# Performance work log

Hardware: AMD Instinct MI355X
Metric: run time of the kernel (lower is better)

The kernel has to match this reference:

```python
import jax, jax.numpy as jnp
import numpy as np


def _gcn_conv(x, edge_index, W, b):
    """Faithful PyG GCNConv: add self-loops, symmetric norm, scatter-sum, bias."""
    n = x.shape[0]
    loop = jnp.arange(n, dtype=edge_index.dtype)
    src = jnp.concatenate([edge_index[0], loop])  # [E+n]
    dst = jnp.concatenate([edge_index[1], loop])
    # in-degree at dst (edge_weight = 1), as in gcn_norm
    deg = jax.ops.segment_sum(jnp.ones(src.shape[0], x.dtype), dst, num_segments=n)
    dinv = jnp.where(deg > 0, jax.lax.rsqrt(deg), 0.0)
    norm = dinv[src] * dinv[dst]                  # [E+n]
    h = x @ W                                     # [n, C] small GEMM
    msg = h[src] * norm[:, None]                  # gather + scale (dominant traffic)
    out = jax.ops.segment_sum(msg, dst, num_segments=n)  # scatter-sum
    return out + b


def setup_inputs() -> dict:
    key = jax.random.key(0)
    ks = jax.random.split(key, 8)
    N, E, C = 50000, 1000000, 64
    scale = 1.0 / np.sqrt(C)
    return {
        "x_star": jax.random.normal(ks[0], (N, C), jnp.float32),
        "x_gal": jax.random.normal(ks[1], (N, C), jnp.float32),
        "edge_ss_near": jax.random.randint(ks[2], (2, E), 0, N, jnp.int64),
        "edge_ss_far": jax.random.randint(ks[3], (2, E), 0, N, jnp.int64),
        "edge_gg_near": jax.random.randint(ks[4], (2, E), 0, N, jnp.int64),
        "W_ss_near": jax.random.normal(ks[5], (C, C), jnp.float32) * scale,
        "W_ss_far": jax.random.normal(ks[6], (C, C), jnp.float32) * scale,
        "W_gg_near": jax.random.normal(ks[7], (C, C), jnp.float32) * scale,
        "b_ss_near": jnp.zeros((C,), jnp.float32),
        "b_ss_far": jnp.zeros((C,), jnp.float32),
        "b_gg_near": jnp.zeros((C,), jnp.float32),
    }


def reference(x_star, x_gal, edge_ss_near, edge_ss_far, edge_gg_near,
              W_ss_near, W_ss_far, W_gg_near,
              b_ss_near, b_ss_far, b_gg_near):
    # HeteroConv with aggr='sum': per-edge-type GCNConv, summed per dst node type.
    out_star = (_gcn_conv(x_star, edge_ss_near, W_ss_near, b_ss_near)
                + _gcn_conv(x_star, edge_ss_far, W_ss_far, b_ss_far))
    out_gal = _gcn_conv(x_gal, edge_gg_near, W_gg_near, b_gg_near)
    return out_star, out_gal
```

## Files before the change

kernel.cpp:

```cpp
#include <hip/hip_runtime.h>
#include <hip/hip_fp16.h>

#define CCH 64
#define RPB 32
#define PCH 4096
#define NBMAX 1568
#define GR 64
#define SG 4
#define STCAP 4096

typedef int int4a __attribute__((ext_vector_type(4), aligned(4)));

__global__ void __launch_bounds__(256) k_hist(const int* __restrict__ e0,
        const int* __restrict__ e1, const int* __restrict__ e2,
        int* __restrict__ H, int E, int NB, int NBLK) {
    int c = blockIdx.y;
    const int* dd = ((c == 0) ? e0 : (c == 1) ? e1 : e2) + E;
    int base = blockIdx.x * PCH;
    int nE = E - base; if (nE > PCH) nE = PCH;
    __shared__ int hist[NBMAX];
    int t = threadIdx.x;
    for (int i = t; i < NB; i += 256) hist[i] = 0;
    __syncthreads();
    for (int k = t * 4; k < nE; k += 1024) {
        if (k + 3 < nE) {
            int4a d = *(const int4a*)(dd + base + k);
            atomicAdd(&hist[d.x >> 5], 1); atomicAdd(&hist[d.y >> 5], 1);
            atomicAdd(&hist[d.z >> 5], 1); atomicAdd(&hist[d.w >> 5], 1);
        } else {
            for (int j = k; j < nE; ++j) atomicAdd(&hist[dd[base + j] >> 5], 1);
        }
    }
    __syncthreads();
    int* Hrow = H + ((size_t)c * NBLK + blockIdx.x) * NB;
    for (int i = t; i < NB; i += 256) Hrow[i] = hist[i];
}

__global__ void __launch_bounds__(256) k_colscan(int* __restrict__ H,
        int* __restrict__ colsum, int NB, int NBLK) {
    int c = blockIdx.y;
    int b = blockIdx.x * 4 + (threadIdx.x >> 6);
    if (b >= NB) return;
    int l = threadIdx.x & 63;
    int* Hc = H + (size_t)c * NBLK * NB;
    int run = 0;
    for (int c0 = 0; c0 < NBLK; c0 += 64) {
        int blk = c0 + l;
        int v = (blk < NBLK) ? Hc[(size_t)blk * NB + b] : 0;
        int s = v;
        #pragma unroll
        for (int off = 1; off < 64; off <<= 1) {
            int u = __shfl_up(s, off, 64);
            if (l >= off) s += u;
        }
        if (blk < NBLK) Hc[(size_t)blk * NB + b] = run + s - v;
        run += __shfl(s, 63, 64);
    }
    if (l == 0) colsum[c * NB + b] = run;
}

__global__ void __launch_bounds__(1024) k_bscan(const int* __restrict__ colsum,
        int* __restrict__ bstart, __half* __restrict__ zrow, int NB, int E) {
    int c = blockIdx.x, t = threadIdx.x;
    if (c == 0 && t < 32) ((float*)zrow)[t] = 0.f;
    __shared__ int sm[1024];
    int i0 = 2 * t, i1 = 2 * t + 1;
    int v0 = (i0 < NB) ? colsum[c * NB + i0] : 0;
    int v1 = (i1 < NB) ? colsum[c * NB + i1] : 0;
    sm[t] = v0 + v1;
    __syncthreads();
    #pragma unroll
    for (int off = 1; off < 1024; off <<= 1) {
        int u = (t >= off) ? sm[t - off] : 0;
        __syncthreads();
        sm[t] += u;
        __syncthreads();
    }
    int ex = sm[t] - (v0 + v1);
    if (i0 < NB) bstart[c * (NB + 1) + i0] = ex;
    if (i1 < NB) bstart[c * (NB + 1) + i1] = ex + v0;
    if (t == 0) bstart[c * (NB + 1) + NB] = E;
}

__global__ void __launch_bounds__(256) k_part2(const int* __restrict__ e0,
        const int* __restrict__ e1, const int* __restrict__ e2,
        const int* __restrict__ H, const int* __restrict__ colsum,
        const int* __restrict__ bstart,
        unsigned* __restrict__ bdata, int E, int NB, int NBLK) {
    int c = blockIdx.y;
    const int* ed = (c == 0) ? e0 : (c == 1) ? e1 : e2;
    int base = blockIdx.x * PCH;
    int nE = E - base; if (nE > PCH) nE = PCH;
    __shared__ unsigned staged[PCH];
    __shared__ int hist[NBMAX];
    __shared__ int off[NBMAX];
    __shared__ int sm[256];
    int t = threadIdx.x;
    const int* Hcur = H + ((size_t)c * NBLK + blockIdx.x) * NB;
    const int* Hnxt = (blockIdx.x == NBLK - 1) ? (colsum + c * NB)
                                               : (Hcur + NB);
    const int* bs = bstart + c * (NB + 1);
    for (int i = t; i < NB; i += 256) {
        int cu = Hcur[i];
        off[i] = bs[i] + cu;
        hist[i] = Hnxt[i] - cu;
    }
    __syncthreads();
    int C = (NB + 255) >> 8;
    int lo = t * C, hi = lo + C; if (hi > NB) hi = NB; if (lo > NB) lo = NB;
    int s = 0;
    for (int i = lo; i < hi; ++i) s += hist[i];
    sm[t] = s;
    __syncthreads();
    #pragma unroll
    for (int o = 1; o < 256; o <<= 1) {
        int u = (t >= o) ? sm[t - o] : 0;
        __syncthreads();
        sm[t] += u;
        __syncthreads();
    }
    int run = (t == 0) ? 0 : sm[t - 1];
    for (int i = lo; i < hi; ++i) {
        int h = hist[i];
        off[i] -= run;
        hist[i] = run;
        run += h;
    }
    __syncthreads();
    for (int k = t * 4; k < nE; k += 1024) {
        if (k + 3 < nE) {
            int4a s4 = *(const int4a*)(ed + base + k);
            int4a d4 = *(const int4a*)(ed + E + base + k);
            int sl;
            sl = atomicAdd(&hist[d4.x >> 5], 1); staged[sl] = (unsigned)s4.x | ((unsigned)d4.x << 16);
            sl = atomicAdd(&hist[d4.y >> 5], 1); staged[sl] = (unsigned)s4.y | ((unsigned)d4.y << 16);
            sl = atomicAdd(&hist[d4.z >> 5], 1); staged[sl] = (unsigned)s4.z | ((unsigned)d4.z << 16);
            sl = atomicAdd(&hist[d4.w >> 5], 1); staged[sl] = (unsigned)s4.w | ((unsigned)d4.w << 16);
        } else {
            for (int j = k; j < nE; ++j) {
                int s0 = ed[base + j];
                int d0 = ed[E + base + j];
                int sl = atomicAdd(&hist[d0 >> 5], 1);
                staged[sl] = (unsigned)s0 | ((unsigned)d0 << 16);
            }
        }
    }
    __syncthreads();
    unsigned* bo = bdata + (size_t)c * E;
    for (int sI = t; sI < nE; sI += 256) {
        unsigned rec = staged[sI];
        int b = (int)(rec >> 16) >> 5;
        bo[off[b] + sI] = rec;
    }
}

__global__ void __launch_bounds__(256) k_sort32(const unsigned* __restrict__ bdata,
        const int* __restrict__ bstart, int* __restrict__ sdat,
        int* __restrict__ rs, float* __restrict__ dinv, int E, int N, int NB) {
    int c = blockIdx.y;
    int b0 = blockIdx.x * SG;
    __shared__ unsigned staged[STCAP];
    __shared__ int cnt[SG * RPB];
    __shared__ int cur[SG * RPB];
    __shared__ int sb[SG + 1];
    int t = threadIdx.x;
    if (t < SG * RPB) cnt[t] = 0;
    if (t <= SG) {
        int b = b0 + t; if (b > NB) b = NB;
        sb[t] = bstart[c * (NB + 1) + b];
    }
    __syncthreads();
    int s0 = sb[0], sE = sb[SG];
    int n = sE - s0;
    const unsigned* bd = bdata + (size_t)c * E;
    bool fits = (n <= STCAP);
    if (fits) {
        for (int i = t; i < n; i += 256) staged[i] = bd[s0 + i];
        __syncthreads();
        for (int i = t; i < n; i += 256) {
            int dst = (int)(staged[i] >> 16);
            atomicAdd(&cnt[((dst >> 5) - b0) * RPB + (dst & 31)], 1);
        }
    } else {
        for (int i = s0 + t; i < sE; i += 256) {
            int dst = (int)(bd[i] >> 16);
            atomicAdd(&cnt[((dst >> 5) - b0) * RPB + (dst & 31)], 1);
        }
    }
    __syncthreads();
    if (t < SG * RPB) {
        int v = cnt[t];
        int s = v;
        #pragma unroll
        for (int off = 1; off < RPB; off <<= 1) {
            int u = __shfl_up(s, off, RPB);
            if ((t & (RPB - 1)) >= off) s += u;
        }
        int g = t >> 5, r = t & 31;
        int ex = sb[g] + s - v;
        cur[t] = ex;
        int row = (b0 + g) * RPB + r;
        if (b0 + g < NB && row < N) {
            rs[c * (N + 1) + row] = ex;
            dinv[c * N + row] = rsqrtf((float)(v + 1));
        }
    }
    if (blockIdx.x == 0 && t == 0) rs[c * (N + 1) + N] = E;
    __syncthreads();
    int* so = sdat + (size_t)c * E;
    if (fits) {
        for (int i = t; i < n; i += 256) {
            unsigned r = staged[i];
            int dst = (int)(r >> 16);
            int slot = atomicAdd(&cur[((dst >> 5) - b0) * RPB + (dst & 31)], 1);
            so[slot] = (int)(r & 0xFFFFu);
        }
    } else {
        for (int i = s0 + t; i < sE; i += 256) {
            unsigned r = bd[i];
            int dst = (int)(r >> 16);
            int slot = atomicAdd(&cur[((dst >> 5) - b0) * RPB + (dst & 31)], 1);
            so[slot] = (int)(r & 0xFFFFu);
        }
    }
}

__global__ void __launch_bounds__(256) k_gemm_all(const float* __restrict__ xs_,
        const float* __restrict__ xg_, const float* __restrict__ W0,
        const float* __restrict__ W1, const float* __restrict__ W2,
        const float* __restrict__ dinv, __half* __restrict__ h16, int N) {
    int star = (blockIdx.y == 0);
    const float* x = star ? xs_ : xg_;
    __shared__ float Ws[2][CCH * CCH];
    __shared__ float xT[CCH * (GR + 1)];
    int t = threadIdx.x;
    int row0 = blockIdx.x * GR;
    size_t NC = (size_t)N * CCH;
    if (star) {
        #pragma unroll
        for (int j = 0; j < 4; ++j) {
            int idx = j * 1024 + t * 4;
            *(float4*)(&Ws[0][idx]) = *(const float4*)(W0 + idx);
            *(float4*)(&Ws[1][idx]) = *(const float4*)(W1 + idx);
        }
    } else {
        #pragma unroll
        for (int j = 0; j < 4; ++j) {
            int idx = j * 1024 + t * 4;
            *(float4*)(&Ws[0][idx]) = *(const float4*)(W2 + idx);
        }
    }
    #pragma unroll
    for (int j = 0; j < 4; ++j) {
        int idx = t + j * 256;
        int r = idx >> 4;
        int c0 = (idx & 15) * 4;
        int row = row0 + r;
        float4 v = make_float4(0.f, 0.f, 0.f, 0.f);
        if (row < N) v = *(const float4*)(x + (size_t)row * CCH + c0);
        xT[(c0 + 0) * (GR + 1) + r] = v.x;
        xT[(c0 + 1) * (GR + 1) + r] = v.y;
        xT[(c0 + 2) * (GR + 1) + r] = v.z;
        xT[(c0 + 3) * (GR + 1) + r] = v.w;
    }
    __syncthreads();
    int c4 = (t & 15) * 4;
    int r0 = (t >> 4) * 4;
    if (star) {
        float4 a0 = make_float4(0.f, 0.f, 0.f, 0.f), a1 = a0, a2 = a0, a3 = a0;
        float4 d0 = a0, d1 = a0, d2 = a0, d3 = a0;
        #pragma unroll 4
        for (int k = 0; k < CCH; ++k) {
            float4 wv = *(float4*)(&Ws[0][k * CCH + c4]);
            float4 uv = *(float4*)(&Ws[1][k * CCH + c4]);
            float x0 = xT[k * (GR + 1) + r0 + 0];
            float x1 = xT[k * (GR + 1) + r0 + 1];
            float x2 = xT[k * (GR + 1) + r0 + 2];
            float x3 = xT[k * (GR + 1) + r0 + 3];
            a0.x += x0 * wv.x; a0.y += x0 * wv.y; a0.z += x0 * wv.z; a0.w += x0 * wv.w;
            a1.x += x1 * wv.x; a1.y += x1 * wv.y; a1.z += x1 * wv.z; a1.w += x1 * wv.w;
            a2.x += x2 * wv.x; a2.y += x2 * wv.y; a2.z += x2 * wv.z; a2.w += x2 * wv.w;
            a3.x += x3 * wv.x; a3.y += x3 * wv.y; a3.z += x3 * wv.z; a3.w += x3 * wv.w;
            d0.x += x0 * uv.x; d0.y += x0 * uv.y; d0.z += x0 * uv.z; d0.w += x0 * uv.w;
            d1.x += x1 * uv.x; d1.y += x1 * uv.y; d1.z += x1 * uv.z; d1.w += x1 * uv.w;
            d2.x += x2 * uv.x; d2.y += x2 * uv.y; d2.z += x2 * uv.z; d2.w += x2 * uv.w;
            d3.x += x3 * uv.x; d3.y += x3 * uv.y; d3.z += x3 * uv.z; d3.w += x3 * uv.w;
        }
        float4 av[4] = {a0, a1, a2, a3};
        float4 dv4[4] = {d0, d1, d2, d3};
        #pragma unroll
        for (int i = 0; i < 4; ++i) {
            int row = row0 + r0 + i;
            if (row < N) {
                float dd0 = dinv[row];
                float dd1 = dinv[N + row];
                union { __half2 h2[2]; float2 f2; } u;
                u.h2[0] = __floats2half2_rn(av[i].x * dd0, av[i].y * dd0);
                u.h2[1] = __floats2half2_rn(av[i].z * dd0, av[i].w * dd0);
                *(float2*)(h16 + (size_t)row * CCH + c4) = u.f2;
                u.h2[0] = __floats2half2_rn(dv4[i].x * dd1, dv4[i].y * dd1);
                u.h2[1] = __floats2half2_rn(dv4[i].z * dd1, dv4[i].w * dd1);
                *(float2*)(h16 + NC + (size_t)row * CCH + c4) = u.f2;
            }
        }
    } else {
        float4 a0 = make_float4(0.f, 0.f, 0.f, 0.f), a1 = a0, a2 = a0, a3 = a0;
        #pragma unroll 8
        for (int k = 0; k < CCH; ++k) {
            float4 wv = *(float4*)(&Ws[0][k * CCH + c4]);
            float x0 = xT[k * (GR + 1) + r0 + 0];
            float x1 = xT[k * (GR + 1) + r0 + 1];
            float x2 = xT[k * (GR + 1) + r0 + 2];
            float x3 = xT[k * (GR + 1) + r0 + 3];
            a0.x += x0 * wv.x; a0.y += x0 * wv.y; a0.z += x0 * wv.z; a0.w += x0 * wv.w;
            a1.x += x1 * wv.x; a1.y += x1 * wv.y; a1.z += x1 * wv.z; a1.w += x1 * wv.w;
            a2.x += x2 * wv.x; a2.y += x2 * wv.y; a2.z += x2 * wv.z; a2.w += x2 * wv.w;
            a3.x += x3 * wv.x; a3.y += x3 * wv.y; a3.z += x3 * wv.z; a3.w += x3 * wv.w;
        }
        float4 av[4] = {a0, a1, a2, a3};
        #pragma unroll
        for (int i = 0; i < 4; ++i) {
            int row = row0 + r0 + i;
            if (row < N) {
                float dd = dinv[2 * N + row];
                union { __half2 h2[2]; float2 f2; } u;
                u.h2[0] = __floats2half2_rn(av[i].x * dd, av[i].y * dd);
                u.h2[1] = __floats2half2_rn(av[i].z * dd, av[i].w * dd);
                *(float2*)(h16 + 2 * NC + (size_t)row * CCH + c4) = u.f2;
            }
        }
    }
}

__device__ __forceinline__ float4 gat4p(const __half* __restrict__ p, int l16) {
    union { float2 f2; __half2 h2[2]; } u;
    u.f2 = ((const float2*)p)[l16];
    float2 a = __half22float2(u.h2[0]);
    float2 b = __half22float2(u.h2[1]);
    return make_float4(a.x, a.y, b.x, b.y);
}

__device__ __forceinline__ void acc4(float4& a, float4 v) {
    a.x += v.x; a.y += v.y; a.z += v.z; a.w += v.w;
}

__global__ void __launch_bounds__(256) k_pull(const int* __restrict__ rs,
        const int* __restrict__ sdat, const __half* __restrict__ h16,
        const float* __restrict__ dinv, const __half* __restrict__ zrow,
        const float* __restrict__ b0, const float* __restrict__ b1,
        const float* __restrict__ b2,
        float* __restrict__ out, int N, int E) {
    int row = blockIdx.x * 4 + (threadIdx.x >> 6);
    if (row >= 2 * N) return;
    int lane = threadIdx.x & 63;
    int q = lane >> 4;
    int l16 = lane & 15;
    size_t NC = (size_t)N * CCH;

    const __half* hcL;
    const int* sdL;
    int beg, end;
    float ddL;
    float4 bias;
    float* op;
    float4 acc = make_float4(0.f, 0.f, 0.f, 0.f);
    if (row < N) {
        int cv = q >> 1;
        const int* rsA = rs + cv * (N + 1);
        int bg = rsA[row], eg = rsA[row + 1];
        int mid = (bg + eg) >> 1;
        beg = (q & 1) ? mid : bg;
        end = (q & 1) ? eg : mid;
        hcL = h16 + (size_t)cv * NC;
        sdL = sdat + (size_t)cv * E;
        ddL = dinv[cv * N + row];
        if (!(q & 1)) acc = gat4p(hcL + (size_t)row * CCH, l16);
        float4 bv0 = ((const float4*)b0)[l16];
        float4 bv1 = ((const float4*)b1)[l16];
        bias = make_float4(bv0.x + bv1.x, bv0.y + bv1.y,
                           bv0.z + bv1.z, bv0.w + bv1.w);
        op = out + (size_t)row * CCH;
    } else {
        int r = row - N;
        const int* rs2 = rs + 2 * (N + 1);
        int bg = rs2[r], eg = rs2[r + 1];
        int len = eg - bg;
        beg = bg + ((len * q) >> 2);
        end = bg + ((len * (q + 1)) >> 2);
        hcL = h16 + 2 * NC;
        sdL = sdat + 2 * (size_t)E;
        ddL = dinv[2 * N + r];
        if (q == 0) acc = gat4p(hcL + (size_t)r * CCH, l16);
        bias = ((const float4*)b2)[l16];
        op = out + NC + (size_t)r * CCH;
    }

    int i = beg;
    for (; i + 7 < end; i += 8) {
        int4a q0 = *(const int4a*)(sdL + i);
        int4a q1 = *(const int4a*)(sdL + i + 4);
        float4 v0 = gat4p(hcL + (size_t)q0.x * CCH, l16);
        float4 v1 = gat4p(hcL + (size_t)q0.y * CCH, l16);
        float4 v2 = gat4p(hcL + (size_t)q0.z * CCH, l16);
        float4 v3 = gat4p(hcL + (size_t)q0.w * CCH, l16);
        float4 v4 = gat4p(hcL + (size_t)q1.x * CCH, l16);
        float4 v5 = gat4p(hcL + (size_t)q1.y * CCH, l16);
        float4 v6 = gat4p(hcL + (size_t)q1.z * CCH, l16);
        float4 v7 = gat4p(hcL + (size_t)q1.w * CCH, l16);
        acc4(acc, v0); acc4(acc, v1); acc4(acc, v2); acc4(acc, v3);
        acc4(acc, v4); acc4(acc, v5); acc4(acc, v6); acc4(acc, v7);
    }
    if (i < end) {
        int4a q0 = *(const int4a*)(sdL + i);
        int4a q1 = *(const int4a*)(sdL + i + 4);
        const __half* p0 = hcL + (size_t)q0.x * CCH;
        const __half* p1 = (i + 1 < end) ? hcL + (size_t)q0.y * CCH : zrow;
        const __half* p2 = (i + 2 < end) ? hcL + (size_t)q0.z * CCH : zrow;
        const __half* p3 = (i + 3 < end) ? hcL + (size_t)q0.w * CCH : zrow;
        const __half* p4 = (i + 4 < end) ? hcL + (size_t)q1.x * CCH : zrow;
        const __half* p5 = (i + 5 < end) ? hcL + (size_t)q1.y * CCH : zrow;
        const __half* p6 = (i + 6 < end) ? hcL + (size_t)q1.z * CCH : zrow;
        const __half* p7 = (i + 7 < end) ? hcL + (size_t)q1.w * CCH : zrow;
        float4 v0 = gat4p(p0, l16);
        float4 v1 = gat4p(p1, l16);
        float4 v2 = gat4p(p2, l16);
        float4 v3 = gat4p(p3, l16);
        float4 v4 = gat4p(p4, l16);
        float4 v5 = gat4p(p5, l16);
        float4 v6 = gat4p(p6, l16);
        float4 v7 = gat4p(p7, l16);
        acc4(acc, v0); acc4(acc, v1); acc4(acc, v2); acc4(acc, v3);
        acc4(acc, v4); acc4(acc, v5); acc4(acc, v6); acc4(acc, v7);
    }

    float4 t;
    t.x = acc.x * ddL; t.y = acc.y * ddL; t.z = acc.z * ddL; t.w = acc.w * ddL;
    t.x += __shfl_xor(t.x, 16, 64); t.y += __shfl_xor(t.y, 16, 64);
    t.z += __shfl_xor(t.z, 16, 64); t.w += __shfl_xor(t.w, 16, 64);
    t.x += __shfl_xor(t.x, 32, 64); t.y += __shfl_xor(t.y, 32, 64);
    t.z += __shfl_xor(t.z, 32, 64); t.w += __shfl_xor(t.w, 32, 64);
    if (lane < 16) {
        t.x += bias.x; t.y += bias.y; t.z += bias.z; t.w += bias.w;
        ((float4*)op)[l16] = t;
    }
}

static inline size_t align256(size_t x) { return (x + 255) & ~(size_t)255; }

extern "C" void kernel_launch(void* const* d_in, const int* in_sizes, int n_in,
                              void* d_out, int out_size, void* d_ws, size_t ws_size,
                              hipStream_t stream) {
    const float* x_star = (const float*)d_in[0];
    const float* x_gal  = (const float*)d_in[1];
    const int*   e_ssn  = (const int*)d_in[2];
    const int*   e_ssf  = (const int*)d_in[3];
    const int*   e_ggn  = (const int*)d_in[4];
    const float* W_ssn  = (const float*)d_in[5];
    const float* W_ssf  = (const float*)d_in[6];
    const float* W_ggn  = (const float*)d_in[7];
    const float* b_ssn  = (const float*)d_in[8];
    const float* b_ssf  = (const float*)d_in[9];
    const float* b_ggn  = (const float*)d_in[10];

    const int N  = in_sizes[0] / CCH;
    const int E  = in_sizes[2] / 2;
    const size_t NC = (size_t)N * CCH;
    const int NB   = (N + RPB - 1) / RPB;
    const int NBLK = (E + PCH - 1) / PCH;

    char* w = (char*)d_ws;
    __half*   h16    = (__half*)w;   w += align256((size_t)3 * NC * 2);
    float*    dinv   = (float*)w;    w += align256((size_t)3 * N * 4);
    unsigned* bdata  = (unsigned*)w; w += align256((size_t)3 * E * 4);
    int*      sdat   = (int*)w;      w += align256((size_t)3 * E * 4);
    int*      H      = (int*)w;      w += align256((size_t)3 * NBLK * NB * 4);
    int*      colsum = (int*)w;      w += align256((size_t)3 * NB * 4);
    int*      bstart = (int*)w;      w += align256((size_t)3 * (NB + 1) * 4);
    int*      rs     = (int*)w;      w += align256((size_t)3 * (N + 1) * 4);
    __half*   zrow   = (__half*)w;   w += align256((size_t)CCH * 2);

    const int B = 256;

    k_hist<<<dim3(NBLK, 3), B, 0, stream>>>(e_ssn, e_ssf, e_ggn, H, E, NB, NBLK);
    k_colscan<<<dim3((NB + 3) / 4, 3), B, 0, stream>>>(H, colsum, NB, NBLK);
    k_bscan<<<3, 1024, 0, stream>>>(colsum, bstart, zrow, NB, E);
    k_part2<<<dim3(NBLK, 3), B, 0, stream>>>(e_ssn, e_ssf, e_ggn, H, colsum,
                                             bstart, bdata, E, NB, NBLK);
    k_sort32<<<dim3((NB + SG - 1) / SG, 3), B, 0, stream>>>(bdata, bstart, sdat,
                                                            rs, dinv, E, N, NB);
    k_gemm_all<<<dim3((N + GR - 1) / GR, 2), B, 0, stream>>>(x_star, x_gal,
                                                             W_ssn, W_ssf, W_ggn,
                                                             dinv, h16, N);
    k_pull<<<(2 * N + 3) / 4, B, 0, stream>>>(rs, sdat, h16, dinv, zrow,
                                              b_ssn, b_ssf, b_ggn,
                                              (float*)d_out, N, E);
}
```

Baseline: 237.7 us.

## Replace two-level bucket sort CSR build with global-atomic counting sort

The multi-kernel CSR construction (per-chunk bucket histograms, column scans, a partition pass and a per-bucket local sort) is replaced by a direct counting sort. Per-row in-degrees are counted with global atomics, scanned into row starts, and each edge's source is then scattered into its slot through global atomic cursors. This drops the intermediate bdata buffer, the large H histogram matrix and two kernel launches. In exchange it relies on heavily contended global atomics and scattered global writes, and the order of edges within a row becomes nondeterministic.

```diff
diff --git a/kernel.cpp b/kernel.cpp
--- a/kernel.cpp
+++ b/kernel.cpp
@@ -3,70 +3,48 @@
 
 #define CCH 64
 #define RPB 32
-#define PCH 4096
-#define NBMAX 1568
+#define PCH 8192
 #define GR 64
-#define SG 4
-#define STCAP 4096
 
 typedef int int4a __attribute__((ext_vector_type(4), aligned(4)));
 
-__global__ void __launch_bounds__(256) k_hist(const int* __restrict__ e0,
+__global__ void __launch_bounds__(256) k_cnt(const int* __restrict__ e0,
         const int* __restrict__ e1, const int* __restrict__ e2,
-        int* __restrict__ H, int E, int NB, int NBLK) {
+        int* __restrict__ rcnt, int E, int N) {
     int c = blockIdx.y;
     const int* dd = ((c == 0) ? e0 : (c == 1) ? e1 : e2) + E;
+    int* rc = rcnt + (size_t)c * N;
     int base = blockIdx.x * PCH;
     int nE = E - base; if (nE > PCH) nE = PCH;
-    __shared__ int hist[NBMAX];
     int t = threadIdx.x;
-    for (int i = t; i < NB; i += 256) hist[i] = 0;
-    __syncthreads();
     for (int k = t * 4; k < nE; k += 1024) {
         if (k + 3 < nE) {
             int4a d = *(const int4a*)(dd + base + k);
-            atomicAdd(&hist[d.x >> 5], 1); atomicAdd(&hist[d.y >> 5], 1);
-            atomicAdd(&hist[d.z >> 5], 1); atomicAdd(&hist[d.w >> 5], 1);
+            atomicAdd(&rc[d.x], 1); atomicAdd(&rc[d.y], 1);
+            atomicAdd(&rc[d.z], 1); atomicAdd(&rc[d.w], 1);
         } else {
-            for (int j = k; j < nE; ++j) atomicAdd(&hist[dd[base + j] >> 5], 1);
-        }
-    }
-    __syncthreads();
-    int* Hrow = H + ((size_t)c * NBLK + blockIdx.x) * NB;
-    for (int i = t; i < NB; i += 256) Hrow[i] = hist[i];
-}
-
-__global__ void __launch_bounds__(256) k_colscan(int* __restrict__ H,
-        int* __restrict__ colsum, int NB, int NBLK) {
-    int c = blockIdx.y;
-    int b = blockIdx.x * 4 + (threadIdx.x >> 6);
-    if (b >= NB) return;
-    int l = threadIdx.x & 63;
-    int* Hc = H + (size_t)c * NBLK * NB;
-    int run = 0;
-    for (int c0 = 0; c0 < NBLK; c0 += 64) {
-        int blk = c0 + l;
-        int v = (blk < NBLK) ? Hc[(size_t)blk * NB + b] : 0;
-        int s = v;
-        #pragma unroll
-        for (int off = 1; off < 64; off <<= 1) {
-            int u = __shfl_up(s, off, 64);
-            if (l >= off) s += u;
-        }
-        if (blk < NBLK) Hc[(size_t)blk * NB + b] = run + s - v;
-        run += __shfl(s, 63, 64);
-    }
-    if (l == 0) colsum[c * NB + b] = run;
-}
-
-__global__ void __launch_bounds__(1024) k_bscan(const int* __restrict__ colsum,
-        int* __restrict__ bstart, __half* __restrict__ zrow, int NB, int E) {
+            for (int j = k; j < nE; ++j) atomicAdd(&rc[dd[base + j]], 1);
+        }
+    }
+}
+
+__global__ void __launch_bounds__(1024) k_bscan(const int* __restrict__ rcnt,
+        int* __restrict__ bstart, __half* __restrict__ zrow,
+        int NB, int N, int E) {
     int c = blockIdx.x, t = threadIdx.x;
     if (c == 0 && t < 32) ((float*)zrow)[t] = 0.f;
     __shared__ int sm[1024];
+    const int* rc = rcnt + (size_t)c * N;
     int i0 = 2 * t, i1 = 2 * t + 1;
-    int v0 = (i0 < NB) ? colsum[c * NB + i0] : 0;
-    int v1 = (i1 < NB) ? colsum[c * NB + i1] : 0;
+    int v0 = 0, v1 = 0;
+    if (i0 < NB) {
+        int r0 = i0 * RPB, hi = r0 + RPB; if (hi > N) hi = N;
+        for (int r = r0; r < hi; ++r) v0 += rc[r];
+    }
+    if (i1 < NB) {
+        int r0 = i1 * RPB, hi = r0 + RPB; if (hi > N) hi = N;
+        for (int r = r0; r < hi; ++r) v1 += rc[r];
+    }
     sm[t] = v0 + v1;
     __syncthreads();
     #pragma unroll
@@ -82,145 +60,53 @@
     if (t == 0) bstart[c * (NB + 1) + NB] = E;
 }
 
-__global__ void __launch_bounds__(256) k_part2(const int* __restrict__ e0,
+__global__ void __launch_bounds__(256) k_rs(const int* __restrict__ rcnt,
+        const int* __restrict__ bstart, int* __restrict__ rs,
+        int* __restrict__ cursor, float* __restrict__ dinv,
+        int N, int NB, int E) {
+    int c = blockIdx.y;
+    int row = blockIdx.x * 256 + threadIdx.x;
+    int l = threadIdx.x & 31;
+    int v = (row < N) ? rcnt[(size_t)c * N + row] : 0;
+    int s = v;
+    #pragma unroll
+    for (int off = 1; off < RPB; off <<= 1) {
+        int u = __shfl_up(s, off, RPB);
+        if (l >= off) s += u;
+    }
+    if (row < N) {
+        int ex = bstart[c * (NB + 1) + (row >> 5)] + s - v;
+        rs[c * (N + 1) + row] = ex;
+        cursor[(size_t)c * N + row] = ex;
+        dinv[(size_t)c * N + row] = rsqrtf((float)(v + 1));
+    }
+    if (blockIdx.x == 0 && threadIdx.x == 0) rs[c * (N + 1) + N] = E;
+}
+
+__global__ void __launch_bounds__(256) k_scat(const int* __restrict__ e0,
         const int* __restrict__ e1, const int* __restrict__ e2,
-        const int* __restrict__ H, const int* __restrict__ colsum,
-        const int* __restrict__ bstart,
-        unsigned* __restrict__ bdata, int E, int NB, int NBLK) {
+        int* __restrict__ cursor, int* __restrict__ sdat, int E, int N) {
     int c = blockIdx.y;
     const int* ed = (c == 0) ? e0 : (c == 1) ? e1 : e2;
+    int* cur = cursor + (size_t)c * N;
+    int* so = sdat + (size_t)c * E;
     int base = blockIdx.x * PCH;
     int nE = E - base; if (nE > PCH) nE = PCH;
-    __shared__ unsigned staged[PCH];
-    __shared__ int hist[NBMAX];
-    __shared__ int off[NBMAX];
-    __shared__ int sm[256];
     int t = threadIdx.x;
-    const int* Hcur = H + ((size_t)c * NBLK + blockIdx.x) * NB;
-    const int* Hnxt = (blockIdx.x == NBLK - 1) ? (colsum + c * NB)
-                                               : (Hcur + NB);
-    const int* bs = bstart + c * (NB + 1);
-    for (int i = t; i < NB; i += 256) {
-        int cu = Hcur[i];
-        off[i] = bs[i] + cu;
-        hist[i] = Hnxt[i] - cu;
-    }
-    __syncthreads();
-    int C = (NB + 255) >> 8;
-    int lo = t * C, hi = lo + C; if (hi > NB) hi = NB; if (lo > NB) lo = NB;
-    int s = 0;
-    for (int i = lo; i < hi; ++i) s += hist[i];
-    sm[t] = s;
-    __syncthreads();
-    #pragma unroll
-    for (int o = 1; o < 256; o <<= 1) {
-        int u = (t >= o) ? sm[t - o] : 0;
-        __syncthreads();
-        sm[t] += u;
-        __syncthreads();
-    }
-    int run = (t == 0) ? 0 : sm[t - 1];
-    for (int i = lo; i < hi; ++i) {
-        int h = hist[i];
-        off[i] -= run;
-        hist[i] = run;
-        run += h;
-    }
-    __syncthreads();
     for (int k = t * 4; k < nE; k += 1024) {
         if (k + 3 < nE) {
             int4a s4 = *(const int4a*)(ed + base + k);
             int4a d4 = *(const int4a*)(ed + E + base + k);
             int sl;
-            sl = atomicAdd(&hist[d4.x >> 5], 1); staged[sl] = (unsigned)s4.x | ((unsigned)d4.x << 16);
-            sl = atomicAdd(&hist[d4.y >> 5], 1); staged[sl] = (unsigned)s4.y | ((unsigned)d4.y << 16);
-            sl = atomicAdd(&hist[d4.z >> 5], 1); staged[sl] = (unsigned)s4.z | ((unsigned)d4.z << 16);
-            sl = atomicAdd(&hist[d4.w >> 5], 1); staged[sl] = (unsigned)s4.w | ((unsigned)d4.w << 16);
+            sl = atomicAdd(&cur[d4.x], 1); so[sl] = s4.x;
+            sl = atomicAdd(&cur[d4.y], 1); so[sl] = s4.y;
+            sl = atomicAdd(&cur[d4.z], 1); so[sl] = s4.z;
+            sl = atomicAdd(&cur[d4.w], 1); so[sl] = s4.w;
         } else {
             for (int j = k; j < nE; ++j) {
-                int s0 = ed[base + j];
-                int d0 = ed[E + base + j];
-                int sl = atomicAdd(&hist[d0 >> 5], 1);
-                staged[sl] = (unsigned)s0 | ((unsigned)d0 << 16);
+                int sl = atomicAdd(&cur[ed[E + base + j]], 1);
+                so[sl] = ed[base + j];
             }
-        }
-    }
-    __syncthreads();
-    unsigned* bo = bdata + (size_t)c * E;
-    for (int sI = t; sI < nE; sI += 256) {
-        unsigned rec = staged[sI];
-        int b = (int)(rec >> 16) >> 5;
-        bo[off[b] + sI] = rec;
-    }
-}
-
-__global__ void __launch_bounds__(256) k_sort32(const unsigned* __restrict__ bdata,
-        const int* __restrict__ bstart, int* __restrict__ sdat,
-        int* __restrict__ rs, float* __restrict__ dinv, int E, int N, int NB) {
-    int c = blockIdx.y;
-    int b0 = blockIdx.x * SG;
-    __shared__ unsigned staged[STCAP];
-    __shared__ int cnt[SG * RPB];
-    __shared__ int cur[SG * RPB];
-    __shared__ int sb[SG + 1];
-    int t = threadIdx.x;
-    if (t < SG * RPB) cnt[t] = 0;
-    if (t <= SG) {
-        int b = b0 + t; if (b > NB) b = NB;
-        sb[t] = bstart[c * (NB + 1) + b];
-    }
-    __syncthreads();
-    int s0 = sb[0], sE = sb[SG];
-    int n = sE - s0;
-    const unsigned* bd = bdata + (size_t)c * E;
-    bool fits = (n <= STCAP);
-    if (fits) {
-        for (int i = t; i < n; i += 256) staged[i] = bd[s0 + i];
-        __syncthreads();
-        for (int i = t; i < n; i += 256) {
-            int dst = (int)(staged[i] >> 16);
-            atomicAdd(&cnt[((dst >> 5) - b0) * RPB + (dst & 31)], 1);
-        }
-    } else {
-        for (int i = s0 + t; i < sE; i += 256) {
-            int dst = (int)(bd[i] >> 16);
-            atomicAdd(&cnt[((dst >> 5) - b0) * RPB + (dst & 31)], 1);
-        }
-    }
-    __syncthreads();
-    if (t < SG * RPB) {
-        int v = cnt[t];
-        int s = v;
-        #pragma unroll
-        for (int off = 1; off < RPB; off <<= 1) {
-            int u = __shfl_up(s, off, RPB);
-            if ((t & (RPB - 1)) >= off) s += u;
-        }
-        int g = t >> 5, r = t & 31;
-        int ex = sb[g] + s - v;
-        cur[t] = ex;
-        int row = (b0 + g) * RPB + r;
-        if (b0 + g < NB && row < N) {
-            rs[c * (N + 1) + row] = ex;
-            dinv[c * N + row] = rsqrtf((float)(v + 1));
-        }
-    }
-    if (blockIdx.x == 0 && t == 0) rs[c * (N + 1) + N] = E;
-    __syncthreads();
-    int* so = sdat + (size_t)c * E;
-    if (fits) {
-        for (int i = t; i < n; i += 256) {
-            unsigned r = staged[i];
-            int dst = (int)(r >> 16);
-            int slot = atomicAdd(&cur[((dst >> 5) - b0) * RPB + (dst & 31)], 1);
-            so[slot] = (int)(r & 0xFFFFu);
-        }
-    } else {
-        for (int i = s0 + t; i < sE; i += 256) {
-            unsigned r = bd[i];
-            int dst = (int)(r >> 16);
-            int slot = atomicAdd(&cur[((dst >> 5) - b0) * RPB + (dst & 31)], 1);
-            so[slot] = (int)(r & 0xFFFFu);
         }
     }
 }
@@ -471,23 +357,21 @@
     char* w = (char*)d_ws;
     __half*   h16    = (__half*)w;   w += align256((size_t)3 * NC * 2);
     float*    dinv   = (float*)w;    w += align256((size_t)3 * N * 4);
-    unsigned* bdata  = (unsigned*)w; w += align256((size_t)3 * E * 4);
     int*      sdat   = (int*)w;      w += align256((size_t)3 * E * 4);
-    int*      H      = (int*)w;      w += align256((size_t)3 * NBLK * NB * 4);
-    int*      colsum = (int*)w;      w += align256((size_t)3 * NB * 4);
+    int*      rcnt   = (int*)w;      w += align256((size_t)3 * N * 4);
+    int*      cursor = (int*)w;      w += align256((size_t)3 * N * 4);
     int*      bstart = (int*)w;      w += align256((size_t)3 * (NB + 1) * 4);
     int*      rs     = (int*)w;      w += align256((size_t)3 * (N + 1) * 4);
     __half*   zrow   = (__half*)w;   w += align256((size_t)CCH * 2);
 
     const int B = 256;
 
-    k_hist<<<dim3(NBLK, 3), B, 0, stream>>>(e_ssn, e_ssf, e_ggn, H, E, NB, NBLK);
-    k_colscan<<<dim3((NB + 3) / 4, 3), B, 0, stream>>>(H, colsum, NB, NBLK);
-    k_bscan<<<3, 1024, 0, stream>>>(colsum, bstart, zrow, NB, E);
-    k_part2<<<dim3(NBLK, 3), B, 0, stream>>>(e_ssn, e_ssf, e_ggn, H, colsum,
-                                             bstart, bdata, E, NB, NBLK);
-    k_sort32<<<dim3((NB + SG - 1) / SG, 3), B, 0, stream>>>(bdata, bstart, sdat,
-                                                            rs, dinv, E, N, NB);
+    hipMemsetAsync(rcnt, 0, (size_t)3 * N * 4, stream);
+    k_cnt<<<dim3(NBLK, 3), B, 0, stream>>>(e_ssn, e_ssf, e_ggn, rcnt, E, N);
+    k_bscan<<<3, 1024, 0, stream>>>(rcnt, bstart, zrow, NB, N, E);
+    k_rs<<<dim3((N + 255) / 256, 3), B, 0, stream>>>(rcnt, bstart, rs, cursor,
+                                                     dinv, N, NB, E);
+    k_scat<<<dim3(NBLK, 3), B, 0, stream>>>(e_ssn, e_ssf, e_ggn, cursor, sdat, E, N);
     k_gemm_all<<<dim3((N + GR - 1) / GR, 2), B, 0, stream>>>(x_star, x_gal,
                                                              W_ssn, W_ssf, W_ggn,
                                                              dinv, h16, N);
```

New measurement: 539.3 us. 127% more time.
